# Kernel tuning notes

Measured on AMD Instinct MI355X. Metric: run time of the kernel, lower is better.

Reference implementation:

```python
import jax, jax.numpy as jnp
import numpy as np
from jax import lax

B, T, D, R, V = 128, 8, 2048, 4, 512

def setup_inputs() -> dict:
    key = jax.random.key(0)
    k0, k1, k2, k3, k4 = jax.random.split(key, 5)
    # scales chosen so the TT products stay within fp32 range (see notes)
    input_embs = jax.random.normal(k0, (B, T, D), dtype=jnp.float32) * 0.1
    label_ids = jax.random.randint(k1, (B, T), 0, V)
    w_alpha = jax.random.normal(k2, (D, R), dtype=jnp.float32) * 0.04
    w_beta = jax.random.normal(k3, (D, R), dtype=jnp.float32) * 0.04
    w_vocab = jax.random.normal(k4, (D, V * R * R), dtype=jnp.float32) * 0.04
    return {"input_embs": input_embs, "label_ids": label_ids,
            "w_alpha": w_alpha, "w_beta": w_beta, "w_vocab": w_vocab}

def _tt_loss(input_embs, w_alpha, w_beta, w_vocab, label_ids):
    b, t, d = input_embs.shape
    flat = input_embs.reshape(-1, d)                    # [B*T, D]
    alpha = jnp.abs((flat @ w_alpha).reshape(b, t, R).mean(1))   # [B, R]
    beta = jnp.abs((flat @ w_beta).reshape(b, t, R).mean(1))     # [B, R]
    core = jnp.abs((flat @ w_vocab).reshape(b, t, R, V, R).mean(1))  # [B, R, V, R]

    # --- _select: gather per-position R x R cores and chain-multiply ---
    core_v = core.transpose(0, 2, 1, 3)                 # [B, V, R, R]
    sel = jnp.take_along_axis(core_v, label_ids[:, :, None, None], axis=1)  # [B, T, R, R]
    sel_t = jnp.swapaxes(sel, 0, 1)                     # [T, B, R, R]

    def chain(carry, m):
        return jnp.einsum('bik,bkj->bij', carry, m), None
    res, _ = lax.scan(chain, sel_t[0], sel_t[1:])       # [B, R, R]
    u = jnp.einsum('bi,bij,bj->b', alpha, res, beta)    # unnormalized probs [B]

    # --- normalization constant: marg^(T+1) contracted with alpha/beta ---
    marg = core.sum(2)                                  # [B, R, R]

    def pow_step(c, _):
        return jnp.einsum('bik,bkj->bij', c, marg), None
    zmat, _ = lax.scan(pow_step, marg, None, length=t)  # marg^(t+1)
    z = jnp.einsum('bi,bij,bj->b', alpha, zmat, beta)

    loss = -jnp.log(u / z)
    return loss.mean()

def reference(input_embs, label_ids, w_alpha, w_beta, w_vocab):
    return _tt_loss(input_embs, w_alpha, w_beta, w_vocab, label_ids)
```

## Files before the change

kernel.cpp:

```cpp
#include <hip/hip_runtime.h>
#include <math.h>

#define BB 128
#define TT 8
#define DD 2048
#define RR 4
#define VV 512

typedef __attribute__((ext_vector_type(8))) short short8;
typedef __attribute__((ext_vector_type(4))) float v4f;

__device__ __forceinline__ unsigned pack_bf16(float x, float y) {
    union { float f; unsigned u; } a, b;
    a.f = x; b.f = y;
    unsigned ua = a.u + 0x7fffu + ((a.u >> 16) & 1u);
    unsigned ub = b.u + 0x7fffu + ((b.u >> 16) & 1u);
    return (ua >> 16) | (ub & 0xffff0000u);
}

__global__ __launch_bounds__(256) void phaseA(const float* __restrict__ inp,
                                              const float* __restrict__ w_alpha,
                                              const float* __restrict__ w_beta,
                                              unsigned short* __restrict__ fmb,
                                              float* __restrict__ alphaP,
                                              float* __restrict__ betaP,
                                              float* __restrict__ marg) {
    int bid = blockIdx.x;
    int b = bid >> 1, half = bid & 1;
    int tid = threadIdx.x;

    if (bid < 8) marg[bid * 256 + tid] = 0.f;

    const float* base = inp + (size_t)b * TT * DD;
    float pa[4] = {0.f, 0.f, 0.f, 0.f};
    float pb[4] = {0.f, 0.f, 0.f, 0.f};
#pragma unroll
    for (int i = 0; i < 4; ++i) {
        int d = half * 1024 + i * 256 + tid;
        float s = 0.f;
#pragma unroll
        for (int t = 0; t < TT; ++t) s += base[t * DD + d];
        float v = s * (1.0f / TT);
        union { float f; unsigned u; } cv; cv.f = v;
        unsigned r = cv.u + 0x7fffu + ((cv.u >> 16) & 1u);
        fmb[b * DD + d] = (unsigned short)(r >> 16);
        float4 wa = *(const float4*)(w_alpha + d * 4);
        float4 wb = *(const float4*)(w_beta + d * 4);
        pa[0] += v * wa.x; pa[1] += v * wa.y; pa[2] += v * wa.z; pa[3] += v * wa.w;
        pb[0] += v * wb.x; pb[1] += v * wb.y; pb[2] += v * wb.z; pb[3] += v * wb.w;
    }
#pragma unroll
    for (int r = 0; r < 4; ++r) {
        for (int m = 1; m < 64; m <<= 1) {
            pa[r] += __shfl_xor(pa[r], m);
            pb[r] += __shfl_xor(pb[r], m);
        }
    }
    __shared__ float sA[4][4], sB[4][4];
    int wid = tid >> 6;
    if ((tid & 63) == 0) {
#pragma unroll
        for (int r = 0; r < 4; ++r) { sA[wid][r] = pa[r]; sB[wid][r] = pb[r]; }
    }
    __syncthreads();
    if (tid < 4) {
        alphaP[b * 8 + half * 4 + tid] = sA[0][tid] + sA[1][tid] + sA[2][tid] + sA[3][tid];
        betaP [b * 8 + half * 4 + tid] = sB[0][tid] + sB[1][tid] + sB[2][tid] + sB[3][tid];
    }
}

__global__ __launch_bounds__(512, 4) void phaseB(const unsigned short* __restrict__ fmb,
                                                 const float* __restrict__ wv,
                                                 const int* __restrict__ labels,
                                                 float* __restrict__ margA,
                                                 float* __restrict__ sel) {
    __shared__ unsigned short Ws[2][16][268];
    __shared__ int slab[BB * TT];

    const int tid = threadIdx.x;
    const int bid = blockIdx.x;
    const int nb = ((bid & 7) << 6) | (bid >> 3);
    const int col0 = nb * 16;

    slab[tid] = labels[tid];
    slab[tid + 512] = labels[tid + 512];

    const int nq = tid & 3;
    const int kp = tid >> 2;
    const int w = tid >> 6;
    const int lane = tid & 63;
    const int m15 = lane & 15;
    const int q = lane >> 4;

    const float* wbase = wv + (size_t)(2 * kp) * 8192 + col0 + nq * 4;
    const unsigned short* abase = fmb + (w * 16 + m15) * DD + q * 8;

    v4f acc = {0.f, 0.f, 0.f, 0.f};
    short8 afrA[8], afrB[8];
    float4 swA0, swA1, swB0, swB1;

    swA0 = *(const float4*)(wbase);
    swA1 = *(const float4*)(wbase + 8192);
    {
        const float* p = wbase + (size_t)256 * 8192;
        swB0 = *(const float4*)(p);
        swB1 = *(const float4*)(p + 8192);
    }
#pragma unroll
    for (int ks = 0; ks < 8; ++ks) afrA[ks] = *(const short8*)(abase + ks * 32);
    {
        const float* f0 = (const float*)&swA0;
        const float* f1 = (const float*)&swA1;
#pragma unroll
        for (int j = 0; j < 4; ++j)
            *(unsigned*)&Ws[0][nq * 4 + j][2 * kp] = pack_bf16(f0[j], f1[j]);
    }
    __syncthreads();

#pragma unroll
    for (int i = 0; i < 4; ++i) {
        const int c0 = 2 * i;
        if (c0 < 6) {
            const float* p = wbase + (size_t)(c0 + 2) * 256 * 8192;
            swA0 = *(const float4*)(p);
            swA1 = *(const float4*)(p + 8192);
        }
        {
            const unsigned short* ap = abase + (c0 + 1) * 256;
#pragma unroll
            for (int ks = 0; ks < 8; ++ks) afrB[ks] = *(const short8*)(ap + ks * 32);
        }
#pragma unroll
        for (int ks = 0; ks < 8; ++ks) {
            short8 b0 = *(const short8*)&Ws[0][m15][ks * 32 + q * 8];
            acc = __builtin_amdgcn_mfma_f32_16x16x32_bf16(afrA[ks], b0, acc, 0, 0, 0);
        }
        {
            const float* f0 = (const float*)&swB0;
            const float* f1 = (const float*)&swB1;
#pragma unroll
            for (int j = 0; j < 4; ++j)
                *(unsigned*)&Ws[1][nq * 4 + j][2 * kp] = pack_bf16(f0[j], f1[j]);
        }
        __syncthreads();

        const int c1 = 2 * i + 1;
        if (c1 < 6) {
            const float* p = wbase + (size_t)(c1 + 2) * 256 * 8192;
            swB0 = *(const float4*)(p);
            swB1 = *(const float4*)(p + 8192);
        }
        if (c1 < 7) {
            const unsigned short* ap = abase + (c1 + 1) * 256;
#pragma unroll
            for (int ks = 0; ks < 8; ++ks) afrA[ks] = *(const short8*)(ap + ks * 32);
        }
#pragma unroll
        for (int ks = 0; ks < 8; ++ks) {
            short8 b1 = *(const short8*)&Ws[1][m15][ks * 32 + q * 8];
            acc = __builtin_amdgcn_mfma_f32_16x16x32_bf16(afrB[ks], b1, acc, 0, 0, 0);
        }
        if (c1 < 7) {
            const float* f0 = (const float*)&swA0;
            const float* f1 = (const float*)&swA1;
#pragma unroll
            for (int j = 0; j < 4; ++j)
                *(unsigned*)&Ws[0][nq * 4 + j][2 * kp] = pack_bf16(f0[j], f1[j]);
        }
        __syncthreads();
    }

    const int i_out = nb >> 7;
    const int j = m15 & 3;
    const int v0 = (nb & 127) * 4 + (m15 >> 2);
    const float* ap = (const float*)&acc;
#pragma unroll
    for (int r = 0; r < 4; ++r) {
        int m = w * 16 + q * 4 + r;
        float a0 = fabsf(ap[r]);
        float s = a0;
        s += __shfl_xor(s, 4);
        s += __shfl_xor(s, 8);
        if ((lane & 12) == 0) atomicAdd(&margA[m * 16 + i_out * 4 + j], s);
#pragma unroll
        for (int t = 0; t < TT; ++t) {
            int lv = slab[m * 8 + t];
            if (lv == v0) sel[(m * 8 + t) * 16 + i_out * 4 + j] = a0;
        }
    }
}

__global__ __launch_bounds__(128) void phaseD(const float* __restrict__ alphaP,
                                              const float* __restrict__ betaP,
                                              const float* __restrict__ marg,
                                              const float* __restrict__ sel,
                                              float* __restrict__ out) {
    int b = threadIdx.x;
    const float* sb = sel + b * TT * 16;
    float res[16], tmp[16], mm[16], zm[16];
#pragma unroll
    for (int e = 0; e < 16; ++e) res[e] = sb[e];
    for (int t = 1; t < TT; ++t) {
        const float* m = sb + t * 16;
#pragma unroll
        for (int i = 0; i < 4; ++i)
#pragma unroll
            for (int jj = 0; jj < 4; ++jj) {
                float s = 0.f;
#pragma unroll
                for (int k = 0; k < 4; ++k) s += res[i * 4 + k] * m[k * 4 + jj];
                tmp[i * 4 + jj] = s;
            }
#pragma unroll
        for (int e = 0; e < 16; ++e) res[e] = tmp[e];
    }
#pragma unroll
    for (int e = 0; e < 16; ++e) { mm[e] = marg[b * 16 + e]; zm[e] = mm[e]; }
    for (int st = 0; st < TT; ++st) {
#pragma unroll
        for (int i = 0; i < 4; ++i)
#pragma unroll
            for (int jj = 0; jj < 4; ++jj) {
                float s = 0.f;
#pragma unroll
                for (int k = 0; k < 4; ++k) s += zm[i * 4 + k] * mm[k * 4 + jj];
                tmp[i * 4 + jj] = s;
            }
#pragma unroll
        for (int e = 0; e < 16; ++e) zm[e] = tmp[e];
    }
    float u = 0.f, z = 0.f;
#pragma unroll
    for (int i = 0; i < 4; ++i) {
        float ai = fabsf(alphaP[b * 8 + i] + alphaP[b * 8 + 4 + i]);
#pragma unroll
        for (int jj = 0; jj < 4; ++jj) {
            float bj = fabsf(betaP[b * 8 + jj] + betaP[b * 8 + 4 + jj]);
            u += ai * res[i * 4 + jj] * bj;
            z += ai * zm[i * 4 + jj] * bj;
        }
    }
    float loss = logf(z) - logf(u);
    __shared__ float red[128];
    red[b] = loss;
    __syncthreads();
    for (int off = 64; off >= 1; off >>= 1) {
        if (b < off) red[b] += red[b + off];
        __syncthreads();
    }
    if (b == 0) out[0] = red[0] * (1.0f / BB);
}

extern "C" void kernel_launch(void* const* d_in, const int* in_sizes, int n_in,
                              void* d_out, int out_size, void* d_ws, size_t ws_size,
                              hipStream_t stream) {
    const float* inp     = (const float*)d_in[0];
    const int*   labels  = (const int*)d_in[1];
    const float* w_alpha = (const float*)d_in[2];
    const float* w_beta  = (const float*)d_in[3];
    const float* wv      = (const float*)d_in[4];
    float* out = (float*)d_out;

    float* ws     = (float*)d_ws;
    float* alphaP = ws;
    float* betaP  = ws + 1024;
    float* marg   = ws + 2048;
    float* sel    = ws + 4096;
    unsigned short* fmb = (unsigned short*)(ws + 20480);

    phaseA<<<256, 256, 0, stream>>>(inp, w_alpha, w_beta, fmb, alphaP, betaP, marg);
    phaseB<<<512, 512, 0, stream>>>(fmb, wv, labels, marg, sel);
    phaseD<<<1, 128, 0, stream>>>(alphaP, betaP, marg, sel, out);
}
```

Baseline: 140.9 us.

## Split GEMM into split-K partial tiles without LDS and add reduction kernel

The wvocab GEMM is restructured so each wave owns a 16-column tile and a quarter of K. It loads weights straight from global into registers, packs them to bf16 as the MFMA A operand, and reuses them across all 8 row tiles of the 128 batch rows, with no LDS staging or barriers. Partial results are written to a large fp32 workspace, and a new phaseC kernel sums the four K-quarters, applies abs, and produces the marginal sums and label-selected cores. This removes LDS traffic and synchronisation, at the cost of an extra kernel launch and a roughly 16 MB partial-result write and read.

```diff
diff --git a/kernel.cpp b/kernel.cpp
--- a/kernel.cpp
+++ b/kernel.cpp
@@ -71,121 +71,109 @@
 
 __global__ __launch_bounds__(512, 4) void phaseB(const unsigned short* __restrict__ fmb,
                                                  const float* __restrict__ wv,
-                                                 const int* __restrict__ labels,
-                                                 float* __restrict__ margA,
-                                                 float* __restrict__ sel) {
-    __shared__ unsigned short Ws[2][16][268];
-    __shared__ int slab[BB * TT];
-
+                                                 float* __restrict__ Cpart) {
     const int tid = threadIdx.x;
     const int bid = blockIdx.x;
-    const int nb = ((bid & 7) << 6) | (bid >> 3);
-    const int col0 = nb * 16;
-
-    slab[tid] = labels[tid];
-    slab[tid + 512] = labels[tid + 512];
-
-    const int nq = tid & 3;
-    const int kp = tid >> 2;
     const int w = tid >> 6;
     const int lane = tid & 63;
     const int m15 = lane & 15;
     const int q = lane >> 4;
 
-    const float* wbase = wv + (size_t)(2 * kp) * 8192 + col0 + nq * 4;
-    const unsigned short* abase = fmb + (w * 16 + m15) * DD + q * 8;
-
-    v4f acc = {0.f, 0.f, 0.f, 0.f};
-    short8 afrA[8], afrB[8];
-    float4 swA0, swA1, swB0, swB1;
-
-    swA0 = *(const float4*)(wbase);
-    swA1 = *(const float4*)(wbase + 8192);
-    {
-        const float* p = wbase + (size_t)256 * 8192;
-        swB0 = *(const float4*)(p);
-        swB1 = *(const float4*)(p + 8192);
-    }
-#pragma unroll
-    for (int ks = 0; ks < 8; ++ks) afrA[ks] = *(const short8*)(abase + ks * 32);
-    {
-        const float* f0 = (const float*)&swA0;
-        const float* f1 = (const float*)&swA1;
-#pragma unroll
-        for (int j = 0; j < 4; ++j)
-            *(unsigned*)&Ws[0][nq * 4 + j][2 * kp] = pack_bf16(f0[j], f1[j]);
+    const int nt  = bid * 2 + (w >> 2);
+    const int qrt = w & 3;
+    const int n0  = nt * 16;
+    const int k0  = qrt * 512;
+
+    const float* wp = wv + (size_t)(k0 + q * 8) * 8192 + n0 + m15;
+    const unsigned short* fb = fmb + (size_t)m15 * DD + k0 + q * 8;
+
+    v4f acc[8];
+#pragma unroll
+    for (int mt = 0; mt < 8; ++mt) acc[mt] = (v4f){0.f, 0.f, 0.f, 0.f};
+
+    float af[8], afn[8];
+#pragma unroll
+    for (int j = 0; j < 8; ++j) af[j] = wp[(size_t)j * 8192];
+
+    for (int c = 0; c < 16; ++c) {
+        if (c < 15) {
+            const float* wn = wp + (size_t)(c + 1) * 32 * 8192;
+#pragma unroll
+            for (int j = 0; j < 8; ++j) afn[j] = wn[(size_t)j * 8192];
+        }
+        short8 afr;
+        unsigned* au = (unsigned*)&afr;
+#pragma unroll
+        for (int p = 0; p < 4; ++p) au[p] = pack_bf16(af[2 * p], af[2 * p + 1]);
+        short8 bfr[8];
+#pragma unroll
+        for (int mt = 0; mt < 8; ++mt)
+            bfr[mt] = *(const short8*)(fb + (size_t)mt * 16 * DD + c * 32);
+#pragma unroll
+        for (int mt = 0; mt < 8; ++mt)
+            acc[mt] = __builtin_amdgcn_mfma_f32_16x16x32_bf16(afr, bfr[mt], acc[mt], 0, 0, 0);
+        if (c < 15) {
+#pragma unroll
+            for (int j = 0; j < 8; ++j) af[j] = afn[j];
+        }
+    }
+
+    float* cb = Cpart + ((size_t)qrt * 8192 + n0) * 128;
+#pragma unroll
+    for (int r = 0; r < 4; ++r) {
+        const int rowoff = (q * 4 + r) * 128;
+#pragma unroll
+        for (int mt = 0; mt < 8; ++mt)
+            cb[rowoff + mt * 16 + m15] = acc[mt][r];
+    }
+}
+
+__global__ __launch_bounds__(256) void phaseC(const float* __restrict__ Cpart,
+                                              const int* __restrict__ labels,
+                                              float* __restrict__ marg,
+                                              float* __restrict__ sel) {
+    const int s = blockIdx.x;
+    const int tid = threadIdx.x;
+    const int i = s >> 6;
+    const int v0 = (s & 63) * 8;
+    __shared__ float Cabs[32][132];
+
+    const int nl = tid >> 3;
+    const int m0 = (tid & 7) * 16;
+    const size_t QS = (size_t)8192 * 128;
+    const float* cp = Cpart + ((size_t)s * 32 + nl) * 128 + m0;
+#pragma unroll
+    for (int g = 0; g < 4; ++g) {
+        float4 a0 = *(const float4*)(cp + g * 4);
+        float4 a1 = *(const float4*)(cp + QS + g * 4);
+        float4 a2 = *(const float4*)(cp + 2 * QS + g * 4);
+        float4 a3 = *(const float4*)(cp + 3 * QS + g * 4);
+        Cabs[nl][m0 + g * 4 + 0] = fabsf(a0.x + a1.x + a2.x + a3.x);
+        Cabs[nl][m0 + g * 4 + 1] = fabsf(a0.y + a1.y + a2.y + a3.y);
+        Cabs[nl][m0 + g * 4 + 2] = fabsf(a0.z + a1.z + a2.z + a3.z);
+        Cabs[nl][m0 + g * 4 + 3] = fabsf(a0.w + a1.w + a2.w + a3.w);
     }
     __syncthreads();
 
-#pragma unroll
-    for (int i = 0; i < 4; ++i) {
-        const int c0 = 2 * i;
-        if (c0 < 6) {
-            const float* p = wbase + (size_t)(c0 + 2) * 256 * 8192;
-            swA0 = *(const float4*)(p);
-            swA1 = *(const float4*)(p + 8192);
-        }
-        {
-            const unsigned short* ap = abase + (c0 + 1) * 256;
-#pragma unroll
-            for (int ks = 0; ks < 8; ++ks) afrB[ks] = *(const short8*)(ap + ks * 32);
-        }
-#pragma unroll
-        for (int ks = 0; ks < 8; ++ks) {
-            short8 b0 = *(const short8*)&Ws[0][m15][ks * 32 + q * 8];
-            acc = __builtin_amdgcn_mfma_f32_16x16x32_bf16(afrA[ks], b0, acc, 0, 0, 0);
-        }
-        {
-            const float* f0 = (const float*)&swB0;
-            const float* f1 = (const float*)&swB1;
+    if (tid < 128) {
+#pragma unroll
+        for (int j = 0; j < 4; ++j) {
+            float sj = 0.f;
+#pragma unroll
+            for (int vv = 0; vv < 8; ++vv) sj += Cabs[vv * 4 + j][tid];
+            atomicAdd(&marg[tid * 16 + i * 4 + j], sj);
+        }
+    }
+
+#pragma unroll
+    for (int p = 0; p < 4; ++p) {
+        const int mt_idx = tid * 4 + p;
+        const int lv = labels[mt_idx];
+        if (lv >= v0 && lv < v0 + 8) {
+            const int nb = (lv - v0) * 4;
 #pragma unroll
             for (int j = 0; j < 4; ++j)
-                *(unsigned*)&Ws[1][nq * 4 + j][2 * kp] = pack_bf16(f0[j], f1[j]);
-        }
-        __syncthreads();
-
-        const int c1 = 2 * i + 1;
-        if (c1 < 6) {
-            const float* p = wbase + (size_t)(c1 + 2) * 256 * 8192;
-            swB0 = *(const float4*)(p);
-            swB1 = *(const float4*)(p + 8192);
-        }
-        if (c1 < 7) {
-            const unsigned short* ap = abase + (c1 + 1) * 256;
-#pragma unroll
-            for (int ks = 0; ks < 8; ++ks) afrA[ks] = *(const short8*)(ap + ks * 32);
-        }
-#pragma unroll
-        for (int ks = 0; ks < 8; ++ks) {
-            short8 b1 = *(const short8*)&Ws[1][m15][ks * 32 + q * 8];
-            acc = __builtin_amdgcn_mfma_f32_16x16x32_bf16(afrB[ks], b1, acc, 0, 0, 0);
-        }
-        if (c1 < 7) {
-            const float* f0 = (const float*)&swA0;
-            const float* f1 = (const float*)&swA1;
-#pragma unroll
-            for (int j = 0; j < 4; ++j)
-                *(unsigned*)&Ws[0][nq * 4 + j][2 * kp] = pack_bf16(f0[j], f1[j]);
-        }
-        __syncthreads();
-    }
-
-    const int i_out = nb >> 7;
-    const int j = m15 & 3;
-    const int v0 = (nb & 127) * 4 + (m15 >> 2);
-    const float* ap = (const float*)&acc;
-#pragma unroll
-    for (int r = 0; r < 4; ++r) {
-        int m = w * 16 + q * 4 + r;
-        float a0 = fabsf(ap[r]);
-        float s = a0;
-        s += __shfl_xor(s, 4);
-        s += __shfl_xor(s, 8);
-        if ((lane & 12) == 0) atomicAdd(&margA[m * 16 + i_out * 4 + j], s);
-#pragma unroll
-        for (int t = 0; t < TT; ++t) {
-            int lv = slab[m * 8 + t];
-            if (lv == v0) sel[(m * 8 + t) * 16 + i_out * 4 + j] = a0;
+                sel[mt_idx * 16 + i * 4 + j] = Cabs[nb + j][mt_idx >> 3];
         }
     }
 }
@@ -267,8 +255,10 @@
     float* marg   = ws + 2048;
     float* sel    = ws + 4096;
     unsigned short* fmb = (unsigned short*)(ws + 20480);
+    float* Cpart  = ws + 151552;
 
     phaseA<<<256, 256, 0, stream>>>(inp, w_alpha, w_beta, fmb, alphaP, betaP, marg);
-    phaseB<<<512, 512, 0, stream>>>(fmb, wv, labels, marg, sel);
+    phaseB<<<256, 512, 0, stream>>>(fmb, wv, Cpart);
+    phaseC<<<256, 256, 0, stream>>>(Cpart, labels, marg, sel);
     phaseD<<<1, 128, 0, stream>>>(alphaP, betaP, marg, sel, out);
 }
```

New measurement: 166.8 us. 1.18x slower.
